# Kernel tuning notes

Measured on AMD Instinct MI355X. Metric: run time of the kernel, lower is better.

The kernel has to match this reference:

```python
import jax, jax.numpy as jnp
import numpy as np

N_NODES = 50000
N_EDGES = 800000
HID = 64
N_GRAPHS = 512
RATIO = 0.5
EPS = 1e-12


def setup_inputs() -> dict:
    key = jax.random.key(0)
    k1, k2, k3, k4, k5 = jax.random.split(key, 5)
    emb = jax.random.normal(k1, (N_NODES, HID), dtype=jnp.float32)
    edge_index = jax.random.randint(k2, (2, N_EDGES), 0, N_NODES, dtype=jnp.int32)
    batch = jnp.sort(jax.random.randint(k3, (N_NODES,), 0, N_GRAPHS, dtype=jnp.int32))
    W1 = jax.random.normal(k4, (2 * HID, 4 * HID), dtype=jnp.float32) * 0.05
    b1 = jnp.zeros((4 * HID,), dtype=jnp.float32)
    W2 = jax.random.normal(k5, (4 * HID, 1), dtype=jnp.float32) * 0.05
    b2 = jnp.zeros((1,), dtype=jnp.float32)
    return {"emb": emb, "edge_index": edge_index, "batch": batch,
            "W1": W1, "b1": b1, "W2": W2, "b2": b2}


def _relabel(edge_index, keep):
    # node_mask[v] = 1 iff v appears as endpoint of any kept edge
    flat = edge_index.reshape(-1)                       # [2E]
    keep2 = jnp.concatenate([keep, keep]).astype(jnp.int32)
    flag = jnp.zeros((N_NODES,), jnp.int32).at[flat].max(keep2)
    node_mask = flag > 0
    # compact new ids (torch: node_idx[sub_nodes] = arange(len(sub_nodes)))
    node_idx = jnp.where(node_mask, jnp.cumsum(node_mask.astype(jnp.int32)) - 1, -1)
    ei_rel = jnp.where(keep[None, :], node_idx[edge_index], -1)  # [2,E], -1 on dropped edges
    return ei_rel


def reference(emb, edge_index, batch, W1, b1, W2, b2):
    row, col = edge_index[0], edge_index[1]
    # edge MLP scoring: cat([emb[row], emb[col]]) -> Linear -> ReLU -> Linear -> scalar
    edge_rep = jnp.concatenate([emb[row], emb[col]], axis=-1)          # [E, 2H]
    h = jax.nn.relu(edge_rep @ W1 + b1)                                # [E, 4H]
    edge_att = (h @ W2 + b2).reshape(-1)                               # [E]

    # --- sparse_topk (descending) over segments index = batch[row] ---
    index = batch[row]                                                 # [E] graph id per edge
    f = edge_att
    fmin, fmax = f.min(), f.max()
    norm = (f - fmin) / (fmax - fmin + EPS) - index.astype(f.dtype)    # (-1)**descending = -1
    perm = jnp.argsort(-norm)                                          # descending sort
    ones = jnp.ones((N_EDGES,), jnp.int32)
    deg = jax.ops.segment_sum(ones, index, num_segments=N_GRAPHS)      # edges per graph
    k = jnp.ceil(RATIO * deg.astype(jnp.float32)).astype(jnp.int32)
    cum = jnp.cumsum(deg)
    start = cum - deg                                                  # start index of each graph block
    seg_sorted = index[perm]
    pos = jnp.arange(N_EDGES, dtype=jnp.int32)
    mask_sorted = (pos - start[seg_sorted]) < k[seg_sorted]            # top-k within each block
    keep = jnp.zeros((N_EDGES,), bool).at[perm].set(mask_sorted)       # causal edges, original order

    causal_edge_weight = jnp.where(keep, edge_att, 0.0)
    spu_edge_weight = jnp.where(keep, 0.0, -edge_att)

    causal_ei_rel = _relabel(edge_index, keep)
    spu_ei_rel = _relabel(edge_index, ~keep)

    scores = jnp.stack([edge_att, causal_edge_weight, spu_edge_weight])  # [3, E]
    return scores, causal_ei_rel, spu_ei_rel
```

## Files before the change

### kernel.cpp

```cpp
#include <hip/hip_runtime.h>
#include <hip/hip_bf16.h>
#include <stdint.h>

#define N_NODES 50000
#define N_EDGES 800000
#define N_GRAPHS 512
#define NSUB 16
#define NBUCK (N_GRAPHS * NSUB)

__device__ __forceinline__ unsigned f2sort(float f) {
    unsigned u = __float_as_uint(f);
    return (u & 0x80000000u) ? ~u : (u | 0x80000000u);
}
__device__ __forceinline__ float sort2f(unsigned u) {
    return __uint_as_float((u & 0x80000000u) ? (u ^ 0x80000000u) : ~u);
}

__global__ __launch_bounds__(256) void k0_count(const int* __restrict__ ei,
                                                const int* __restrict__ batch,
                                                unsigned* __restrict__ subdeg,
                                                int* __restrict__ node_start) {
    __shared__ unsigned hist[NBUCK];
    const int tid = threadIdx.x;
    for (int i = tid; i < NBUCK; i += 256) hist[i] = 0;
    __syncthreads();
    const int e0 = blockIdx.x * 4096;
    #pragma unroll 4
    for (int j = 0; j < 16; ++j) {
        int e = e0 + j * 256 + tid;
        if (e < N_EDGES) {
            int r = ei[e], c = ei[N_EDGES + e];
            atomicAdd(&hist[batch[r] * NSUB + (c >> 12)], 1u);
        }
    }
    #pragma unroll 4
    for (int j = 0; j < 16; ++j) {
        int i = e0 + j * 256 + tid;
        if (i < N_NODES) {
            int b = batch[i];
            if (i == 0) { for (int g2 = 0; g2 <= b; ++g2) node_start[g2] = 0; }
            else { int bp = batch[i - 1]; for (int g2 = bp + 1; g2 <= b; ++g2) node_start[g2] = i; }
            if (i == N_NODES - 1) { for (int g2 = b + 1; g2 <= N_GRAPHS; ++g2) node_start[g2] = N_NODES; }
        }
    }
    __syncthreads();
    for (int i = tid; i < NBUCK; i += 256) {
        unsigned h = hist[i];
        if (h) atomicAdd(&subdeg[i], h);
    }
}

__global__ __launch_bounds__(1024) void k3_scan(const unsigned* __restrict__ subdeg,
                                                unsigned* __restrict__ substart,
                                                unsigned* __restrict__ deg,
                                                unsigned* __restrict__ start,
                                                unsigned* __restrict__ kkv) {
    __shared__ unsigned lds[1024];
    const int t = threadIdx.x;
    unsigned v[8], s = 0;
    #pragma unroll
    for (int j = 0; j < 8; ++j) { v[j] = subdeg[t * 8 + j]; s += v[j]; }
    lds[t] = s;
    for (int off = 1; off < 1024; off <<= 1) {
        __syncthreads();
        unsigned u = (t >= off) ? lds[t - off] : 0u;
        __syncthreads();
        lds[t] += u;
    }
    __syncthreads();
    unsigned run = lds[t] - s;
    #pragma unroll
    for (int j = 0; j < 8; ++j) { substart[t * 8 + j] = run; run += v[j]; }
    if (t == 1023) substart[NBUCK] = lds[1023];
    __syncthreads();
    if (t < N_GRAPHS) {
        unsigned st0 = substart[t * NSUB];
        unsigned d = substart[(t + 1) * NSUB] - st0;
        start[t] = st0;
        deg[t] = d;
        kkv[t] = (d + 1u) >> 1;
    }
}

__global__ __launch_bounds__(256) void k4a_scatter(const int* __restrict__ ei,
                                                   const int* __restrict__ batch,
                                                   const unsigned* __restrict__ substart,
                                                   unsigned* __restrict__ subcursor,
                                                   unsigned* __restrict__ rcbuck,
                                                   unsigned* __restrict__ ebuck) {
    int e = blockIdx.x * 256 + threadIdx.x;
    int r = ei[e], c = ei[N_EDGES + e];
    int b = batch[r] * NSUB + (c >> 12);
    unsigned rank = atomicAdd(&subcursor[b], 1u);
    unsigned pos = substart[b] + rank;
    rcbuck[pos] = (unsigned)r | ((unsigned)c << 16);
    ebuck[pos]  = (unsigned)e;
}

__global__ __launch_bounds__(256) void k1_gemm(const float* __restrict__ emb,
                                               const float* __restrict__ W1,
                                               const float* __restrict__ b1,
                                               float* __restrict__ P,
                                               float* __restrict__ Q) {
    __shared__ float As[64][68];
    __shared__ float Bs[64][128];
    const int tid = threadIdx.x;
    const int v0  = blockIdx.x * 64;
    const int cy  = blockIdx.y;

    if (v0 + 64 <= N_NODES) {
        const float* srcA = emb + (size_t)v0 * 64;
        for (int idx = tid * 4; idx < 4096; idx += 1024) {
            float4 x = *(const float4*)(srcA + idx);
            int r = idx >> 6, k = idx & 63;
            As[k + 0][r] = x.x; As[k + 1][r] = x.y; As[k + 2][r] = x.z; As[k + 3][r] = x.w;
        }
    } else {
        for (int idx = tid * 4; idx < 4096; idx += 1024) {
            int r = idx >> 6, k = idx & 63;
            int v = v0 + r; if (v >= N_NODES) v = N_NODES - 1;
            float4 x = *(const float4*)(emb + (size_t)v * 64 + k);
            As[k + 0][r] = x.x; As[k + 1][r] = x.y; As[k + 2][r] = x.z; As[k + 3][r] = x.w;
        }
    }
    for (int idx = tid * 4; idx < 64 * 128; idx += 1024) {
        int k = idx >> 7, c = idx & 127;
        int jj = cy * 128 + c;
        const float* src = (jj < 256) ? (W1 + (size_t)k * 256 + jj)
                                      : (W1 + (size_t)(64 + k) * 256 + (jj - 256));
        *(float4*)&Bs[k][c] = *(const float4*)src;
    }
    __syncthreads();

    const int cgrp = tid & 31;
    const int rgrp = tid >> 5;
    float acc[8][4];
    #pragma unroll
    for (int r = 0; r < 8; ++r) { acc[r][0]=0.f; acc[r][1]=0.f; acc[r][2]=0.f; acc[r][3]=0.f; }

    #pragma unroll 8
    for (int k = 0; k < 64; ++k) {
        float4 b = *(const float4*)&Bs[k][cgrp * 4];
        const float4* ap = (const float4*)&As[k][rgrp * 8];
        float4 a01 = ap[0], a23 = ap[1];
        float av[8] = {a01.x, a01.y, a01.z, a01.w, a23.x, a23.y, a23.z, a23.w};
        #pragma unroll
        for (int r = 0; r < 8; ++r) {
            acc[r][0] = fmaf(av[r], b.x, acc[r][0]);
            acc[r][1] = fmaf(av[r], b.y, acc[r][1]);
            acc[r][2] = fmaf(av[r], b.z, acc[r][2]);
            acc[r][3] = fmaf(av[r], b.w, acc[r][3]);
        }
    }

    const int jj0 = cy * 128 + cgrp * 4;
    float4 badd = {0.f, 0.f, 0.f, 0.f};
    if (jj0 < 256) badd = *(const float4*)(b1 + jj0);
    #pragma unroll
    for (int r = 0; r < 8; ++r) {
        int v = v0 + rgrp * 8 + r;
        if (v < N_NODES) {
            float4 o = {acc[r][0] + badd.x, acc[r][1] + badd.y,
                        acc[r][2] + badd.z, acc[r][3] + badd.w};
            float* dst = (jj0 < 256) ? (P + (size_t)v * 256 + jj0)
                                     : (Q + (size_t)v * 256 + (jj0 - 256));
            *(float4*)dst = o;
        }
    }
}

__global__ __launch_bounds__(512, 4) void k2_edge(const float* __restrict__ P,
                                                  const float* __restrict__ Q,
                                                  const unsigned* __restrict__ rcbuck,
                                                  const unsigned* __restrict__ ebuck,
                                                  const unsigned* __restrict__ deg,
                                                  const unsigned* __restrict__ start,
                                                  const int* __restrict__ node_start,
                                                  const float* __restrict__ W2,
                                                  const float* __restrict__ b2,
                                                  float* __restrict__ att,
                                                  unsigned* __restrict__ minmax,
                                                  int ldsrows) {
    extern __shared__ float4 lds4[];
    const int g = blockIdx.x;
    const int n = (int)deg[g];
    if (n == 0) return;
    const int st = (int)start[g];
    const int n0 = node_start[g];
    const int nr = node_start[g + 1] - n0;
    const int ncap = nr < ldsrows ? nr : ldsrows;
    const int tid = threadIdx.x;

    const float4* Pg4 = (const float4*)(P + (size_t)n0 * 256);
    for (int u = tid; u < ncap * 64; u += 512) lds4[u] = Pg4[u];
    __syncthreads();

    const int lane = tid & 63;
    const int w = tid >> 6;
    const int j0 = lane * 4;
    const float4 w2v = *(const float4*)(W2 + j0);
    const float b2v = b2[0];
    float vmin = __builtin_inff(), vmax = -__builtin_inff();

    const int noct = (n + 7) >> 3;
    for (int oi = w; oi < noct; oi += 8) {
        const int i0 = st + oi * 8;
        int cnt = n - oi * 8; if (cnt > 8) cnt = 8;
        uint4 rcA = *(const uint4*)(rcbuck + i0);
        uint4 rcB = *(const uint4*)(rcbuck + i0 + 4);
        uint4 evA = *(const uint4*)(ebuck + i0);
        uint4 evB = *(const uint4*)(ebuck + i0 + 4);
        unsigned rc[8] = {rcA.x, rcA.y, rcA.z, rcA.w, rcB.x, rcB.y, rcB.z, rcB.w};
        unsigned ev[8] = {evA.x, evA.y, evA.z, evA.w, evB.x, evB.y, evB.z, evB.w};

        float4 p[8], q[8];
        #pragma unroll
        for (int j = 0; j < 8; ++j) {
            int r = (int)(rc[j] & 0xFFFFu);
            int c = (int)(rc[j] >> 16);
            int rl = r - n0;
            q[j] = *(const float4*)(Q + (size_t)c * 256 + j0);
            p[j] = (rl < ncap && rl >= 0) ? lds4[rl * 64 + lane]
                                          : *(const float4*)(P + (size_t)r * 256 + j0);
        }

        float part[8];
        #pragma unroll
        for (int j = 0; j < 8; ++j) {
            float s0 = fmaxf(p[j].x + q[j].x, 0.f);
            float s1 = fmaxf(p[j].y + q[j].y, 0.f);
            float s2 = fmaxf(p[j].z + q[j].z, 0.f);
            float s3 = fmaxf(p[j].w + q[j].w, 0.f);
            part[j] = fmaf(s3, w2v.w, fmaf(s2, w2v.z, fmaf(s1, w2v.y, s0 * w2v.x)));
        }
        #pragma unroll
        for (int off = 32; off; off >>= 1) {
            #pragma unroll
            for (int j = 0; j < 8; ++j) part[j] += __shfl_xor(part[j], off, 64);
        }
        float av = part[0]; unsigned ew = ev[0];
        #pragma unroll
        for (int j = 1; j < 8; ++j) if (lane == j) { av = part[j]; ew = ev[j]; }
        if (lane < cnt) att[ew] = av + b2v;

        #pragma unroll
        for (int j = 0; j < 8; ++j) {
            if (j < cnt) {
                float a = part[j] + b2v;
                vmin = fminf(vmin, a); vmax = fmaxf(vmax, a);
            }
        }
    }
    if (lane == 0) {
        atomicMin(&minmax[0], f2sort(vmin));
        atomicMax(&minmax[1], f2sort(vmax));
    }
}

__global__ __launch_bounds__(256) void k5_select(const unsigned* __restrict__ deg,
                                                 const unsigned* __restrict__ start,
                                                 const unsigned* __restrict__ kk,
                                                 const float* __restrict__ att,
                                                 const unsigned* __restrict__ ebuck,
                                                 const unsigned* __restrict__ rcbuck,
                                                 const unsigned* __restrict__ minmax,
                                                 unsigned char* __restrict__ keep,
                                                 unsigned char* __restrict__ flagC,
                                                 unsigned char* __restrict__ flagS) {
    __shared__ unsigned kbuf[4096];
    __shared__ unsigned hist[256];
    __shared__ unsigned sh_b, sh_excl, sh_cnt;
    const int g = blockIdx.x, t = threadIdx.x;
    int n = (int)deg[g]; if (n > 4096) n = 4096;
    if (n == 0) return;
    const unsigned st = start[g];
    const float fmin = sort2f(minmax[0]);
    const float fmax = sort2f(minmax[1]);
    const float denom = (fmax - fmin) + 1e-12f;
    const float gf = (float)g;
    for (int i = t; i < n; i += 256) {
        float a = att[ebuck[st + i]];
        float nq = (a - fmin) / denom;
        float mq = nq - gf;
        kbuf[i] = ~f2sort(mq);
    }
    const unsigned K = kk[g];

    unsigned lo = 0, prefix = 0, meq = 0;
    for (int byte = 3; byte >= 0; --byte) {
        __syncthreads();
        hist[t] = 0;
        __syncthreads();
        const int shAbove = (byte + 1) * 8;
        for (int i = t; i < n; i += 256) {
            unsigned k = kbuf[i];
            bool ok = (byte == 3) || ((k >> shAbove) == (prefix >> shAbove));
            if (ok) atomicAdd(&hist[(k >> (byte * 8)) & 0xFFu], 1u);
        }
        __syncthreads();
        unsigned v = hist[t];
        for (int off = 1; off < 256; off <<= 1) {
            __syncthreads();
            unsigned u = (t >= off) ? hist[t - off] : 0u;
            __syncthreads();
            hist[t] += u;
        }
        __syncthreads();
        unsigned incl = hist[t], excl = incl - v;
        unsigned target = K - lo;
        if (excl < target && target <= incl) { sh_b = (unsigned)t; sh_excl = excl; sh_cnt = v; }
        __syncthreads();
        prefix |= sh_b << (byte * 8);
        lo += sh_excl;
        meq = sh_cnt;
    }
    const unsigned T32 = prefix;
    const unsigned tneed = K - lo;
    bool keepAllTies = (tneed == meq);

    unsigned E_t = 0xFFFFFFFFu;
    if (!keepAllTies) {
        unsigned elo = 0, eprefix = 0;
        for (int byte = 2; byte >= 0; --byte) {
            __syncthreads();
            hist[t] = 0;
            __syncthreads();
            const int shAbove = (byte + 1) * 8;
            for (int i = t; i < n; i += 256) {
                if (kbuf[i] == T32) {
                    unsigned e = ebuck[st + i];
                    bool ok = (byte == 2) || ((e >> shAbove) == (eprefix >> shAbove));
                    if (ok) atomicAdd(&hist[(e >> (byte * 8)) & 0xFFu], 1u);
                }
            }
            __syncthreads();
            unsigned v = hist[t];
            for (int off = 1; off < 256; off <<= 1) {
                __syncthreads();
                unsigned u = (t >= off) ? hist[t - off] : 0u;
                __syncthreads();
                hist[t] += u;
            }
            __syncthreads();
            unsigned incl = hist[t], excl = incl - v;
            unsigned target = tneed - elo;
            if (excl < target && target <= incl) { sh_b = (unsigned)t; sh_excl = excl; }
            __syncthreads();
            eprefix |= sh_b << (byte * 8);
            elo += sh_excl;
        }
        E_t = eprefix;
    }

    __syncthreads();
    for (int i = t; i < n; i += 256) {
        unsigned k = kbuf[i];
        unsigned e = ebuck[st + i];
        bool kp = (k < T32) || (k == T32 && (keepAllTies || e <= E_t));
        keep[e] = kp ? 1 : 0;
        unsigned rc = rcbuck[st + i];
        int r = (int)(rc & 0xFFFFu), c = (int)(rc >> 16);
        if (kp) { flagC[r] = 1; flagC[c] = 1; }
        else    { flagS[r] = 1; flagS[c] = 1; }
    }
}

__global__ __launch_bounds__(1024) void k7_nodescan(const unsigned char* __restrict__ flagC,
                                                    const unsigned char* __restrict__ flagS,
                                                    int* __restrict__ nidxC,
                                                    int* __restrict__ nidxS) {
    const unsigned char* fl = blockIdx.x ? flagS : flagC;
    int* nx = blockIdx.x ? nidxS : nidxC;
    __shared__ int lds[1024];
    const int t = threadIdx.x;
    const int CH = (N_NODES + 1023) / 1024;
    const int base = t * CH;
    int s = 0;
    for (int i = 0; i < CH; ++i) { int v = base + i; if (v < N_NODES) s += fl[v]; }
    lds[t] = s;
    for (int off = 1; off < 1024; off <<= 1) {
        __syncthreads();
        int v = (t >= off) ? lds[t - off] : 0;
        __syncthreads();
        lds[t] += v;
    }
    __syncthreads();
    int run = lds[t] - s;
    for (int i = 0; i < CH; ++i) {
        int v = base + i;
        if (v < N_NODES) {
            if (fl[v]) { nx[v] = run; run++; } else nx[v] = -1;
        }
    }
}

__global__ __launch_bounds__(256) void k8_out(const float* __restrict__ att,
                                              const unsigned char* __restrict__ keep,
                                              const int* __restrict__ ei,
                                              const int* __restrict__ nidxC,
                                              const int* __restrict__ nidxS,
                                              float* __restrict__ out) {
    int e = blockIdx.x * 256 + threadIdx.x;
    float a = att[e];
    int kp = keep[e];
    int r = ei[e], c = ei[N_EDGES + e];
    out[e]               = a;
    out[N_EDGES + e]     = kp ? a : 0.f;
    out[2 * N_EDGES + e] = kp ? 0.f : -a;
    if (kp) {
        out[3 * N_EDGES + e] = (float)nidxC[r];
        out[4 * N_EDGES + e] = (float)nidxC[c];
        out[5 * N_EDGES + e] = -1.f;
        out[6 * N_EDGES + e] = -1.f;
    } else {
        out[3 * N_EDGES + e] = -1.f;
        out[4 * N_EDGES + e] = -1.f;
        out[5 * N_EDGES + e] = (float)nidxS[r];
        out[6 * N_EDGES + e] = (float)nidxS[c];
    }
}

extern "C" void kernel_launch(void* const* d_in, const int* in_sizes, int n_in,
                              void* d_out, int out_size, void* d_ws, size_t ws_size,
                              hipStream_t stream) {
    const float* emb   = (const float*)d_in[0];
    const int*   ei    = (const int*)d_in[1];
    const int*   batch = (const int*)d_in[2];
    const float* W1    = (const float*)d_in[3];
    const float* b1    = (const float*)d_in[4];
    const float* W2    = (const float*)d_in[5];
    const float* b2    = (const float*)d_in[6];
    float* out = (float*)d_out;

    char* ws = (char*)d_ws;
    size_t off = 0;
    auto alloc = [&](size_t bytes) -> void* {
        off = (off + 255) & ~(size_t)255;
        void* p = ws + off;
        off += bytes;
        return p;
    };

    float* P              = (float*)alloc((size_t)N_NODES * 256 * 4);
    float* Q              = (float*)alloc((size_t)N_NODES * 256 * 4);
    float* att            = (float*)alloc((size_t)N_EDGES * 4);
    unsigned* rcbuck      = (unsigned*)alloc(((size_t)N_EDGES + 8) * 4);
    unsigned* ebuck       = (unsigned*)alloc(((size_t)N_EDGES + 8) * 4);
    unsigned char* keep   = (unsigned char*)alloc(N_EDGES);
    unsigned char* flags2 = (unsigned char*)alloc((size_t)2 * N_NODES);
    unsigned char* flagC  = flags2;
    unsigned char* flagS  = flags2 + N_NODES;
    int* nidxC            = (int*)alloc((size_t)N_NODES * 4);
    int* nidxS            = (int*)alloc((size_t)N_NODES * 4);
    unsigned* meta        = (unsigned*)alloc((2 * NBUCK + 3 * 512 + 2) * 4);
    unsigned* subdeg      = meta;
    unsigned* subcursor   = meta + NBUCK;
    unsigned* deg         = meta + 2 * NBUCK;
    unsigned* start       = meta + 2 * NBUCK + 512;
    unsigned* kk          = meta + 2 * NBUCK + 1024;
    unsigned* minmax      = meta + 2 * NBUCK + 1536;
    unsigned* substart    = (unsigned*)alloc((NBUCK + 1) * 4);
    int* node_start       = (int*)alloc(513 * 4);

    const int EB = (N_EDGES + 255) / 256;
    const int SB = (N_EDGES + 4095) / 4096;

    hipMemsetAsync(meta, 0, (2 * NBUCK + 3 * 512 + 2) * 4, stream);
    hipMemsetAsync(minmax, 0xFF, 4, stream);
    hipMemsetAsync(flags2, 0, (size_t)2 * N_NODES, stream);

    int ldsrows = 78;
    if (hipFuncSetAttribute((const void*)k2_edge,
                            hipFuncAttributeMaxDynamicSharedMemorySize,
                            78 * 1024) != hipSuccess) {
        ldsrows = 56;
    }
    const size_t shbytes = (size_t)ldsrows * 1024;

    k0_count<<<SB, 256, 0, stream>>>(ei, batch, subdeg, node_start);
    k3_scan<<<1, 1024, 0, stream>>>(subdeg, substart, deg, start, kk);
    k4a_scatter<<<EB, 256, 0, stream>>>(ei, batch, substart, subcursor, rcbuck, ebuck);

    dim3 g1((N_NODES + 63) / 64, 4);
    k1_gemm<<<g1, 256, 0, stream>>>(emb, W1, b1, P, Q);

    k2_edge<<<N_GRAPHS, 512, shbytes, stream>>>(P, Q, rcbuck, ebuck, deg, start,
                                                node_start, W2, b2, att, minmax, ldsrows);

    k5_select<<<N_GRAPHS, 256, 0, stream>>>(deg, start, kk, att, ebuck, rcbuck,
                                            minmax, keep, flagC, flagS);
    k7_nodescan<<<2, 1024, 0, stream>>>(flagC, flagS, nidxC, nidxS);
    k8_out<<<EB, 256, 0, stream>>>(att, keep, ei, nidxC, nidxS, out);
}
```

Measured before the change: 407.6 us.

## Fuse count/scan/scatter and select/nodescan/output into persistent grid-barrier kernels

Merges the count, scan and scatter kernels into one kernel, and the select, node-scan and output kernels into another. Both use software grid barriers built on atomic counters, which cuts kernel launches and spreads the node scan across many blocks instead of two. It relies on every block being co-resident (196 and 512 blocks of 256 threads) without a cooperative launch, so it can deadlock if the GPU cannot schedule all blocks at once. It also resets the min/max inside the kernel rather than with a memset.

```diff
diff --git a/kernel.cpp b/kernel.cpp
--- a/kernel.cpp
+++ b/kernel.cpp
@@ -16,15 +16,35 @@
     return __uint_as_float((u & 0x80000000u) ? (u ^ 0x80000000u) : ~u);
 }
 
-__global__ __launch_bounds__(256) void k0_count(const int* __restrict__ ei,
-                                                const int* __restrict__ batch,
-                                                unsigned* __restrict__ subdeg,
-                                                int* __restrict__ node_start) {
+__device__ __forceinline__ void gridbar(unsigned* ctr, unsigned target) {
+    __syncthreads();
+    if (threadIdx.x == 0) {
+        __threadfence();
+        atomicAdd(ctr, 1u);
+        while (__hip_atomic_load(ctr, __ATOMIC_ACQUIRE, __HIP_MEMORY_SCOPE_AGENT) < target)
+            __builtin_amdgcn_s_sleep(2);
+    }
+    __syncthreads();
+}
+
+__global__ __launch_bounds__(256) void coopA(const int* __restrict__ ei,
+                                             const int* __restrict__ batch,
+                                             unsigned* __restrict__ subdeg,
+                                             unsigned* __restrict__ subcursor,
+                                             unsigned* __restrict__ substart,
+                                             int* __restrict__ node_start,
+                                             unsigned* __restrict__ minmax,
+                                             unsigned* __restrict__ bar,
+                                             unsigned* __restrict__ rcbuck,
+                                             unsigned* __restrict__ ebuck) {
     __shared__ unsigned hist[NBUCK];
+    __shared__ unsigned part[256];
     const int tid = threadIdx.x;
+    const int b   = blockIdx.x;
+    const int e0  = b * 4096;
+
     for (int i = tid; i < NBUCK; i += 256) hist[i] = 0;
     __syncthreads();
-    const int e0 = blockIdx.x * 4096;
     #pragma unroll 4
     for (int j = 0; j < 16; ++j) {
         int e = e0 + j * 256 + tid;
@@ -37,10 +57,10 @@
     for (int j = 0; j < 16; ++j) {
         int i = e0 + j * 256 + tid;
         if (i < N_NODES) {
-            int b = batch[i];
-            if (i == 0) { for (int g2 = 0; g2 <= b; ++g2) node_start[g2] = 0; }
-            else { int bp = batch[i - 1]; for (int g2 = bp + 1; g2 <= b; ++g2) node_start[g2] = i; }
-            if (i == N_NODES - 1) { for (int g2 = b + 1; g2 <= N_GRAPHS; ++g2) node_start[g2] = N_NODES; }
+            int bb = batch[i];
+            if (i == 0) { for (int g2 = 0; g2 <= bb; ++g2) node_start[g2] = 0; }
+            else { int bp = batch[i - 1]; for (int g2 = bp + 1; g2 <= bb; ++g2) node_start[g2] = i; }
+            if (i == N_NODES - 1) { for (int g2 = bb + 1; g2 <= N_GRAPHS; ++g2) node_start[g2] = N_NODES; }
         }
     }
     __syncthreads();
@@ -48,53 +68,42 @@
         unsigned h = hist[i];
         if (h) atomicAdd(&subdeg[i], h);
     }
-}
-
-__global__ __launch_bounds__(1024) void k3_scan(const unsigned* __restrict__ subdeg,
-                                                unsigned* __restrict__ substart,
-                                                unsigned* __restrict__ deg,
-                                                unsigned* __restrict__ start,
-                                                unsigned* __restrict__ kkv) {
-    __shared__ unsigned lds[1024];
-    const int t = threadIdx.x;
-    unsigned v[8], s = 0;
-    #pragma unroll
-    for (int j = 0; j < 8; ++j) { v[j] = subdeg[t * 8 + j]; s += v[j]; }
-    lds[t] = s;
-    for (int off = 1; off < 1024; off <<= 1) {
+    if (b == 0 && tid == 0) { minmax[0] = 0xFFFFFFFFu; minmax[1] = 0u; }
+    gridbar(bar + 0, gridDim.x);
+
+    if (b == 0) {
+        unsigned s = 0;
+        for (int j = 0; j < 32; ++j) s += subdeg[tid * 32 + j];
+        part[tid] = s;
+        for (int off = 1; off < 256; off <<= 1) {
+            __syncthreads();
+            unsigned u = (tid >= off) ? part[tid - off] : 0u;
+            __syncthreads();
+            part[tid] += u;
+        }
         __syncthreads();
-        unsigned u = (t >= off) ? lds[t - off] : 0u;
-        __syncthreads();
-        lds[t] += u;
-    }
-    __syncthreads();
-    unsigned run = lds[t] - s;
-    #pragma unroll
-    for (int j = 0; j < 8; ++j) { substart[t * 8 + j] = run; run += v[j]; }
-    if (t == 1023) substart[NBUCK] = lds[1023];
-    __syncthreads();
-    if (t < N_GRAPHS) {
-        unsigned st0 = substart[t * NSUB];
-        unsigned d = substart[(t + 1) * NSUB] - st0;
-        start[t] = st0;
-        deg[t] = d;
-        kkv[t] = (d + 1u) >> 1;
-    }
-}
-
-__global__ __launch_bounds__(256) void k4a_scatter(const int* __restrict__ ei,
-                                                   const int* __restrict__ batch,
-                                                   const unsigned* __restrict__ substart,
-                                                   unsigned* __restrict__ subcursor,
-                                                   unsigned* __restrict__ rcbuck,
-                                                   unsigned* __restrict__ ebuck) {
-    int e = blockIdx.x * 256 + threadIdx.x;
-    int r = ei[e], c = ei[N_EDGES + e];
-    int b = batch[r] * NSUB + (c >> 12);
-    unsigned rank = atomicAdd(&subcursor[b], 1u);
-    unsigned pos = substart[b] + rank;
-    rcbuck[pos] = (unsigned)r | ((unsigned)c << 16);
-    ebuck[pos]  = (unsigned)e;
+        unsigned run = part[tid] - s;
+        for (int j = 0; j < 32; ++j) {
+            unsigned d = subdeg[tid * 32 + j];
+            substart[tid * 32 + j] = run;
+            run += d;
+        }
+        if (tid == 255) substart[NBUCK] = run;
+    }
+    gridbar(bar + 1, gridDim.x);
+
+    #pragma unroll 4
+    for (int j = 0; j < 16; ++j) {
+        int e = e0 + j * 256 + tid;
+        if (e < N_EDGES) {
+            int r = ei[e], c = ei[N_EDGES + e];
+            int bk = batch[r] * NSUB + (c >> 12);
+            unsigned rank = atomicAdd(&subcursor[bk], 1u);
+            unsigned pos = substart[bk] + rank;
+            rcbuck[pos] = (unsigned)r | ((unsigned)c << 16);
+            ebuck[pos]  = (unsigned)e;
+        }
+    }
 }
 
 __global__ __launch_bounds__(256) void k1_gemm(const float* __restrict__ emb,
@@ -173,8 +182,7 @@
                                                   const float* __restrict__ Q,
                                                   const unsigned* __restrict__ rcbuck,
                                                   const unsigned* __restrict__ ebuck,
-                                                  const unsigned* __restrict__ deg,
-                                                  const unsigned* __restrict__ start,
+                                                  const unsigned* __restrict__ substart,
                                                   const int* __restrict__ node_start,
                                                   const float* __restrict__ W2,
                                                   const float* __restrict__ b2,
@@ -183,9 +191,9 @@
                                                   int ldsrows) {
     extern __shared__ float4 lds4[];
     const int g = blockIdx.x;
-    const int n = (int)deg[g];
+    const int st = (int)substart[g * NSUB];
+    const int n = (int)substart[(g + 1) * NSUB] - st;
     if (n == 0) return;
-    const int st = (int)start[g];
     const int n0 = node_start[g];
     const int nr = node_start[g + 1] - n0;
     const int ncap = nr < ldsrows ? nr : ldsrows;
@@ -257,166 +265,175 @@
     }
 }
 
-__global__ __launch_bounds__(256) void k5_select(const unsigned* __restrict__ deg,
-                                                 const unsigned* __restrict__ start,
-                                                 const unsigned* __restrict__ kk,
-                                                 const float* __restrict__ att,
-                                                 const unsigned* __restrict__ ebuck,
-                                                 const unsigned* __restrict__ rcbuck,
-                                                 const unsigned* __restrict__ minmax,
-                                                 unsigned char* __restrict__ keep,
-                                                 unsigned char* __restrict__ flagC,
-                                                 unsigned char* __restrict__ flagS) {
+__global__ __launch_bounds__(256) void coopB(const unsigned* __restrict__ substart,
+                                             const float* __restrict__ att,
+                                             const unsigned* __restrict__ ebuck,
+                                             const unsigned* __restrict__ rcbuck,
+                                             const unsigned* __restrict__ minmax,
+                                             const int* __restrict__ ei,
+                                             unsigned char* __restrict__ keep,
+                                             unsigned char* __restrict__ flagC,
+                                             unsigned char* __restrict__ flagS,
+                                             int* __restrict__ nidxC,
+                                             int* __restrict__ nidxS,
+                                             unsigned* __restrict__ partial,
+                                             unsigned* __restrict__ bar,
+                                             float* __restrict__ out) {
     __shared__ unsigned kbuf[4096];
     __shared__ unsigned hist[256];
     __shared__ unsigned sh_b, sh_excl, sh_cnt;
     const int g = blockIdx.x, t = threadIdx.x;
-    int n = (int)deg[g]; if (n > 4096) n = 4096;
-    if (n == 0) return;
-    const unsigned st = start[g];
-    const float fmin = sort2f(minmax[0]);
-    const float fmax = sort2f(minmax[1]);
-    const float denom = (fmax - fmin) + 1e-12f;
-    const float gf = (float)g;
-    for (int i = t; i < n; i += 256) {
-        float a = att[ebuck[st + i]];
-        float nq = (a - fmin) / denom;
-        float mq = nq - gf;
-        kbuf[i] = ~f2sort(mq);
-    }
-    const unsigned K = kk[g];
-
-    unsigned lo = 0, prefix = 0, meq = 0;
-    for (int byte = 3; byte >= 0; --byte) {
+    const unsigned st = substart[g * NSUB];
+    int n = (int)(substart[(g + 1) * NSUB] - st); if (n > 4096) n = 4096;
+
+    if (n > 0) {
+        const float fmin = sort2f(minmax[0]);
+        const float fmax = sort2f(minmax[1]);
+        const float denom = (fmax - fmin) + 1e-12f;
+        const float gf = (float)g;
+        for (int i = t; i < n; i += 256) {
+            float a = att[ebuck[st + i]];
+            float nq = (a - fmin) / denom;
+            float mq = nq - gf;
+            kbuf[i] = ~f2sort(mq);
+        }
+        const unsigned K = ((unsigned)n + 1u) >> 1;
+
+        unsigned lo = 0, prefix = 0, meq = 0;
+        for (int byte = 3; byte >= 0; --byte) {
+            __syncthreads();
+            hist[t] = 0;
+            __syncthreads();
+            const int shAbove = (byte + 1) * 8;
+            for (int i = t; i < n; i += 256) {
+                unsigned k = kbuf[i];
+                bool ok = (byte == 3) || ((k >> shAbove) == (prefix >> shAbove));
+                if (ok) atomicAdd(&hist[(k >> (byte * 8)) & 0xFFu], 1u);
+            }
+            __syncthreads();
+            unsigned v = hist[t];
+            for (int off = 1; off < 256; off <<= 1) {
+                __syncthreads();
+                unsigned u = (t >= off) ? hist[t - off] : 0u;
+                __syncthreads();
+                hist[t] += u;
+            }
+            __syncthreads();
+            unsigned incl = hist[t], excl = incl - v;
+            unsigned target = K - lo;
+            if (excl < target && target <= incl) { sh_b = (unsigned)t; sh_excl = excl; sh_cnt = v; }
+            __syncthreads();
+            prefix |= sh_b << (byte * 8);
+            lo += sh_excl;
+            meq = sh_cnt;
+        }
+        const unsigned T32 = prefix;
+        const unsigned tneed = K - lo;
+        bool keepAllTies = (tneed == meq);
+
+        unsigned E_t = 0xFFFFFFFFu;
+        if (!keepAllTies) {
+            unsigned elo = 0, eprefix = 0;
+            for (int byte = 2; byte >= 0; --byte) {
+                __syncthreads();
+                hist[t] = 0;
+                __syncthreads();
+                const int shAbove = (byte + 1) * 8;
+                for (int i = t; i < n; i += 256) {
+                    if (kbuf[i] == T32) {
+                        unsigned e = ebuck[st + i];
+                        bool ok = (byte == 2) || ((e >> shAbove) == (eprefix >> shAbove));
+                        if (ok) atomicAdd(&hist[(e >> (byte * 8)) & 0xFFu], 1u);
+                    }
+                }
+                __syncthreads();
+                unsigned v = hist[t];
+                for (int off = 1; off < 256; off <<= 1) {
+                    __syncthreads();
+                    unsigned u = (t >= off) ? hist[t - off] : 0u;
+                    __syncthreads();
+                    hist[t] += u;
+                }
+                __syncthreads();
+                unsigned incl = hist[t], excl = incl - v;
+                unsigned target = tneed - elo;
+                if (excl < target && target <= incl) { sh_b = (unsigned)t; sh_excl = excl; }
+                __syncthreads();
+                eprefix |= sh_b << (byte * 8);
+                elo += sh_excl;
+            }
+            E_t = eprefix;
+        }
+
         __syncthreads();
-        hist[t] = 0;
-        __syncthreads();
-        const int shAbove = (byte + 1) * 8;
         for (int i = t; i < n; i += 256) {
             unsigned k = kbuf[i];
-            bool ok = (byte == 3) || ((k >> shAbove) == (prefix >> shAbove));
-            if (ok) atomicAdd(&hist[(k >> (byte * 8)) & 0xFFu], 1u);
-        }
+            unsigned e = ebuck[st + i];
+            bool kp = (k < T32) || (k == T32 && (keepAllTies || e <= E_t));
+            keep[e] = kp ? 1 : 0;
+            unsigned rc = rcbuck[st + i];
+            int r = (int)(rc & 0xFFFFu), c = (int)(rc >> 16);
+            if (kp) { flagC[r] = 1; flagC[c] = 1; }
+            else    { flagS[r] = 1; flagS[c] = 1; }
+        }
+    }
+    gridbar(bar + 0, gridDim.x);
+
+    const int half = g >> 8;
+    const int bloc = g & 255;
+    const unsigned char* fl = half ? flagS : flagC;
+    int* nx = half ? nidxS : nidxC;
+    const int base = bloc * 196;
+    const int v = base + t;
+    const int f = (t < 196 && v < N_NODES) ? (int)fl[v] : 0;
+    __syncthreads();
+    hist[t] = (unsigned)f;
+    for (int off = 1; off < 256; off <<= 1) {
         __syncthreads();
-        unsigned v = hist[t];
-        for (int off = 1; off < 256; off <<= 1) {
-            __syncthreads();
-            unsigned u = (t >= off) ? hist[t - off] : 0u;
-            __syncthreads();
-            hist[t] += u;
-        }
+        unsigned u = (t >= off) ? hist[t - off] : 0u;
         __syncthreads();
-        unsigned incl = hist[t], excl = incl - v;
-        unsigned target = K - lo;
-        if (excl < target && target <= incl) { sh_b = (unsigned)t; sh_excl = excl; sh_cnt = v; }
+        hist[t] += u;
+    }
+    __syncthreads();
+    const unsigned exclL = hist[t] - (unsigned)f;
+    const unsigned totalMine = hist[255];
+    if (t == 0) partial[g] = totalMine;
+    gridbar(bar + 1, gridDim.x);
+
+    unsigned pv = partial[half * 256 + t];
+    __syncthreads();
+    hist[t] = pv;
+    for (int off = 1; off < 256; off <<= 1) {
         __syncthreads();
-        prefix |= sh_b << (byte * 8);
-        lo += sh_excl;
-        meq = sh_cnt;
-    }
-    const unsigned T32 = prefix;
-    const unsigned tneed = K - lo;
-    bool keepAllTies = (tneed == meq);
-
-    unsigned E_t = 0xFFFFFFFFu;
-    if (!keepAllTies) {
-        unsigned elo = 0, eprefix = 0;
-        for (int byte = 2; byte >= 0; --byte) {
-            __syncthreads();
-            hist[t] = 0;
-            __syncthreads();
-            const int shAbove = (byte + 1) * 8;
-            for (int i = t; i < n; i += 256) {
-                if (kbuf[i] == T32) {
-                    unsigned e = ebuck[st + i];
-                    bool ok = (byte == 2) || ((e >> shAbove) == (eprefix >> shAbove));
-                    if (ok) atomicAdd(&hist[(e >> (byte * 8)) & 0xFFu], 1u);
-                }
-            }
-            __syncthreads();
-            unsigned v = hist[t];
-            for (int off = 1; off < 256; off <<= 1) {
-                __syncthreads();
-                unsigned u = (t >= off) ? hist[t - off] : 0u;
-                __syncthreads();
-                hist[t] += u;
-            }
-            __syncthreads();
-            unsigned incl = hist[t], excl = incl - v;
-            unsigned target = tneed - elo;
-            if (excl < target && target <= incl) { sh_b = (unsigned)t; sh_excl = excl; }
-            __syncthreads();
-            eprefix |= sh_b << (byte * 8);
-            elo += sh_excl;
-        }
-        E_t = eprefix;
-    }
-
-    __syncthreads();
-    for (int i = t; i < n; i += 256) {
-        unsigned k = kbuf[i];
-        unsigned e = ebuck[st + i];
-        bool kp = (k < T32) || (k == T32 && (keepAllTies || e <= E_t));
-        keep[e] = kp ? 1 : 0;
-        unsigned rc = rcbuck[st + i];
-        int r = (int)(rc & 0xFFFFu), c = (int)(rc >> 16);
-        if (kp) { flagC[r] = 1; flagC[c] = 1; }
-        else    { flagS[r] = 1; flagS[c] = 1; }
-    }
-}
-
-__global__ __launch_bounds__(1024) void k7_nodescan(const unsigned char* __restrict__ flagC,
-                                                    const unsigned char* __restrict__ flagS,
-                                                    int* __restrict__ nidxC,
-                                                    int* __restrict__ nidxS) {
-    const unsigned char* fl = blockIdx.x ? flagS : flagC;
-    int* nx = blockIdx.x ? nidxS : nidxC;
-    __shared__ int lds[1024];
-    const int t = threadIdx.x;
-    const int CH = (N_NODES + 1023) / 1024;
-    const int base = t * CH;
-    int s = 0;
-    for (int i = 0; i < CH; ++i) { int v = base + i; if (v < N_NODES) s += fl[v]; }
-    lds[t] = s;
-    for (int off = 1; off < 1024; off <<= 1) {
+        unsigned u = (t >= off) ? hist[t - off] : 0u;
         __syncthreads();
-        int v = (t >= off) ? lds[t - off] : 0;
-        __syncthreads();
-        lds[t] += v;
-    }
-    __syncthreads();
-    int run = lds[t] - s;
-    for (int i = 0; i < CH; ++i) {
-        int v = base + i;
-        if (v < N_NODES) {
-            if (fl[v]) { nx[v] = run; run++; } else nx[v] = -1;
-        }
-    }
-}
-
-__global__ __launch_bounds__(256) void k8_out(const float* __restrict__ att,
-                                              const unsigned char* __restrict__ keep,
-                                              const int* __restrict__ ei,
-                                              const int* __restrict__ nidxC,
-                                              const int* __restrict__ nidxS,
-                                              float* __restrict__ out) {
-    int e = blockIdx.x * 256 + threadIdx.x;
-    float a = att[e];
-    int kp = keep[e];
-    int r = ei[e], c = ei[N_EDGES + e];
-    out[e]               = a;
-    out[N_EDGES + e]     = kp ? a : 0.f;
-    out[2 * N_EDGES + e] = kp ? 0.f : -a;
-    if (kp) {
-        out[3 * N_EDGES + e] = (float)nidxC[r];
-        out[4 * N_EDGES + e] = (float)nidxC[c];
-        out[5 * N_EDGES + e] = -1.f;
-        out[6 * N_EDGES + e] = -1.f;
-    } else {
-        out[3 * N_EDGES + e] = -1.f;
-        out[4 * N_EDGES + e] = -1.f;
-        out[5 * N_EDGES + e] = (float)nidxS[r];
-        out[6 * N_EDGES + e] = (float)nidxS[c];
+        hist[t] += u;
+    }
+    __syncthreads();
+    const unsigned baseOff = hist[bloc] - totalMine;
+    if (t < 196 && v < N_NODES) nx[v] = f ? (int)(baseOff + exclL) : -1;
+    gridbar(bar + 2, gridDim.x);
+
+    const int eb0 = g * 1563;
+    int eend = eb0 + 1563; if (eend > N_EDGES) eend = N_EDGES;
+    for (int e = eb0 + t; e < eend; e += 256) {
+        float a = att[e];
+        int kp = keep[e];
+        int r = ei[e], c = ei[N_EDGES + e];
+        out[e]               = a;
+        out[N_EDGES + e]     = kp ? a : 0.f;
+        out[2 * N_EDGES + e] = kp ? 0.f : -a;
+        if (kp) {
+            out[3 * N_EDGES + e] = (float)nidxC[r];
+            out[4 * N_EDGES + e] = (float)nidxC[c];
+            out[5 * N_EDGES + e] = -1.f;
+            out[6 * N_EDGES + e] = -1.f;
+        } else {
+            out[3 * N_EDGES + e] = -1.f;
+            out[4 * N_EDGES + e] = -1.f;
+            out[5 * N_EDGES + e] = (float)nidxS[r];
+            out[6 * N_EDGES + e] = (float)nidxS[c];
+        }
     }
 }
 
@@ -452,21 +469,18 @@
     unsigned char* flagS  = flags2 + N_NODES;
     int* nidxC            = (int*)alloc((size_t)N_NODES * 4);
     int* nidxS            = (int*)alloc((size_t)N_NODES * 4);
-    unsigned* meta        = (unsigned*)alloc((2 * NBUCK + 3 * 512 + 2) * 4);
+    unsigned* meta        = (unsigned*)alloc((2 * NBUCK + 2 + 8 + 512) * 4);
     unsigned* subdeg      = meta;
     unsigned* subcursor   = meta + NBUCK;
-    unsigned* deg         = meta + 2 * NBUCK;
-    unsigned* start       = meta + 2 * NBUCK + 512;
-    unsigned* kk          = meta + 2 * NBUCK + 1024;
-    unsigned* minmax      = meta + 2 * NBUCK + 1536;
+    unsigned* minmax      = meta + 2 * NBUCK;
+    unsigned* bar         = meta + 2 * NBUCK + 2;
+    unsigned* partial     = meta + 2 * NBUCK + 10;
     unsigned* substart    = (unsigned*)alloc((NBUCK + 1) * 4);
     int* node_start       = (int*)alloc(513 * 4);
 
-    const int EB = (N_EDGES + 255) / 256;
     const int SB = (N_EDGES + 4095) / 4096;
 
-    hipMemsetAsync(meta, 0, (2 * NBUCK + 3 * 512 + 2) * 4, stream);
-    hipMemsetAsync(minmax, 0xFF, 4, stream);
+    hipMemsetAsync(meta, 0, (2 * NBUCK + 2 + 8 + 512) * 4, stream);
     hipMemsetAsync(flags2, 0, (size_t)2 * N_NODES, stream);
 
     int ldsrows = 78;
@@ -477,18 +491,16 @@
     }
     const size_t shbytes = (size_t)ldsrows * 1024;
 
-    k0_count<<<SB, 256, 0, stream>>>(ei, batch, subdeg, node_start);
-    k3_scan<<<1, 1024, 0, stream>>>(subdeg, substart, deg, start, kk);
-    k4a_scatter<<<EB, 256, 0, stream>>>(ei, batch, substart, subcursor, rcbuck, ebuck);
+    coopA<<<SB, 256, 0, stream>>>(ei, batch, subdeg, subcursor, substart,
+                                  node_start, minmax, bar, rcbuck, ebuck);
 
     dim3 g1((N_NODES + 63) / 64, 4);
     k1_gemm<<<g1, 256, 0, stream>>>(emb, W1, b1, P, Q);
 
-    k2_edge<<<N_GRAPHS, 512, shbytes, stream>>>(P, Q, rcbuck, ebuck, deg, start,
+    k2_edge<<<N_GRAPHS, 512, shbytes, stream>>>(P, Q, rcbuck, ebuck, substart,
                                                 node_start, W2, b2, att, minmax, ldsrows);
 
-    k5_select<<<N_GRAPHS, 256, 0, stream>>>(deg, start, kk, att, ebuck, rcbuck,
-                                            minmax, keep, flagC, flagS);
-    k7_nodescan<<<2, 1024, 0, stream>>>(flagC, flagS, nidxC, nidxS);
-    k8_out<<<EB, 256, 0, stream>>>(att, keep, ei, nidxC, nidxS, out);
-}
+    coopB<<<N_GRAPHS, 256, 0, stream>>>(substart, att, ebuck, rcbuck, minmax, ei,
+                                        keep, flagC, flagS, nidxC, nidxS,
+                                        partial, bar + 4, out);
+}
```

New measurement: 583.4 us. 1.43x slower.

## Fold scan into count kernel and merge scatter with GEMM launch

Applied to the files above, without the earlier changes.

The bucket prefix scan now runs in the last-finishing block of the count kernel, detected with an atomic done counter, so the separate scan kernel is gone. The edge scatter shares one launch with the node GEMM: extra blocks past the GEMM range do the scatter, so the two independent jobs can overlap. The three memsets become one, and per-graph degree, start and k are derived from substart inside the consumer kernels. This cuts launch count and small-kernel serialisation, at the cost of a last-block pattern that relies on threadfence ordering.

```diff
diff --git a/kernel.cpp b/kernel.cpp
--- a/kernel.cpp
+++ b/kernel.cpp
@@ -7,6 +7,8 @@
 #define N_GRAPHS 512
 #define NSUB 16
 #define NBUCK (N_GRAPHS * NSUB)
+#define GEMM_BLOCKS 3128
+#define SCAT_BLOCKS 196
 
 __device__ __forceinline__ unsigned f2sort(float f) {
     unsigned u = __float_as_uint(f);
@@ -19,12 +21,17 @@
 __global__ __launch_bounds__(256) void k0_count(const int* __restrict__ ei,
                                                 const int* __restrict__ batch,
                                                 unsigned* __restrict__ subdeg,
-                                                int* __restrict__ node_start) {
+                                                unsigned* __restrict__ substart,
+                                                int* __restrict__ node_start,
+                                                unsigned* __restrict__ minmax,
+                                                unsigned* __restrict__ donecnt) {
     __shared__ unsigned hist[NBUCK];
+    __shared__ unsigned part[256];
+    __shared__ unsigned sh_last;
     const int tid = threadIdx.x;
+    const int e0 = blockIdx.x * 4096;
     for (int i = tid; i < NBUCK; i += 256) hist[i] = 0;
     __syncthreads();
-    const int e0 = blockIdx.x * 4096;
     #pragma unroll 4
     for (int j = 0; j < 16; ++j) {
         int e = e0 + j * 256 + tid;
@@ -48,65 +55,73 @@
         unsigned h = hist[i];
         if (h) atomicAdd(&subdeg[i], h);
     }
-}
-
-__global__ __launch_bounds__(1024) void k3_scan(const unsigned* __restrict__ subdeg,
-                                                unsigned* __restrict__ substart,
-                                                unsigned* __restrict__ deg,
-                                                unsigned* __restrict__ start,
-                                                unsigned* __restrict__ kkv) {
-    __shared__ unsigned lds[1024];
-    const int t = threadIdx.x;
-    unsigned v[8], s = 0;
-    #pragma unroll
-    for (int j = 0; j < 8; ++j) { v[j] = subdeg[t * 8 + j]; s += v[j]; }
-    lds[t] = s;
-    for (int off = 1; off < 1024; off <<= 1) {
-        __syncthreads();
-        unsigned u = (t >= off) ? lds[t - off] : 0u;
-        __syncthreads();
-        lds[t] += u;
-    }
-    __syncthreads();
-    unsigned run = lds[t] - s;
-    #pragma unroll
-    for (int j = 0; j < 8; ++j) { substart[t * 8 + j] = run; run += v[j]; }
-    if (t == 1023) substart[NBUCK] = lds[1023];
-    __syncthreads();
-    if (t < N_GRAPHS) {
-        unsigned st0 = substart[t * NSUB];
-        unsigned d = substart[(t + 1) * NSUB] - st0;
-        start[t] = st0;
-        deg[t] = d;
-        kkv[t] = (d + 1u) >> 1;
-    }
-}
-
-__global__ __launch_bounds__(256) void k4a_scatter(const int* __restrict__ ei,
-                                                   const int* __restrict__ batch,
-                                                   const unsigned* __restrict__ substart,
-                                                   unsigned* __restrict__ subcursor,
-                                                   unsigned* __restrict__ rcbuck,
-                                                   unsigned* __restrict__ ebuck) {
-    int e = blockIdx.x * 256 + threadIdx.x;
-    int r = ei[e], c = ei[N_EDGES + e];
-    int b = batch[r] * NSUB + (c >> 12);
-    unsigned rank = atomicAdd(&subcursor[b], 1u);
-    unsigned pos = substart[b] + rank;
-    rcbuck[pos] = (unsigned)r | ((unsigned)c << 16);
-    ebuck[pos]  = (unsigned)e;
-}
-
-__global__ __launch_bounds__(256) void k1_gemm(const float* __restrict__ emb,
-                                               const float* __restrict__ W1,
-                                               const float* __restrict__ b1,
-                                               float* __restrict__ P,
-                                               float* __restrict__ Q) {
+    if (tid == 0) {
+        minmax[0] = 0xFFFFFFFFu;
+        minmax[1] = 0u;
+        __threadfence();
+        sh_last = atomicAdd(donecnt, 1u);
+    }
+    __syncthreads();
+    if (sh_last != SCAT_BLOCKS - 1) return;
+    __threadfence();
+
+    unsigned v = 0;
+    {
+        unsigned s = 0;
+        unsigned loc[32];
+        #pragma unroll
+        for (int j = 0; j < 32; ++j) { loc[j] = subdeg[tid * 32 + j]; s += loc[j]; }
+        part[tid] = s;
+        for (int off = 1; off < 256; off <<= 1) {
+            __syncthreads();
+            unsigned u = (tid >= off) ? part[tid - off] : 0u;
+            __syncthreads();
+            part[tid] += u;
+        }
+        __syncthreads();
+        unsigned run = part[tid] - s;
+        #pragma unroll
+        for (int j = 0; j < 32; ++j) { substart[tid * 32 + j] = run; run += loc[j]; }
+        if (tid == 255) substart[NBUCK] = run;
+        v = run;
+    }
+    (void)v;
+}
+
+__global__ __launch_bounds__(256) void k14_gemm_scatter(const float* __restrict__ emb,
+                                                        const float* __restrict__ W1,
+                                                        const float* __restrict__ b1,
+                                                        float* __restrict__ P,
+                                                        float* __restrict__ Q,
+                                                        const int* __restrict__ ei,
+                                                        const int* __restrict__ batch,
+                                                        const unsigned* __restrict__ substart,
+                                                        unsigned* __restrict__ subcursor,
+                                                        unsigned* __restrict__ rcbuck,
+                                                        unsigned* __restrict__ ebuck) {
     __shared__ float As[64][68];
     __shared__ float Bs[64][128];
     const int tid = threadIdx.x;
-    const int v0  = blockIdx.x * 64;
-    const int cy  = blockIdx.y;
+
+    if (blockIdx.x >= GEMM_BLOCKS) {
+        const int e0 = (blockIdx.x - GEMM_BLOCKS) * 4096;
+        #pragma unroll 4
+        for (int j = 0; j < 16; ++j) {
+            int e = e0 + j * 256 + tid;
+            if (e < N_EDGES) {
+                int r = ei[e], c = ei[N_EDGES + e];
+                int bk = batch[r] * NSUB + (c >> 12);
+                unsigned rank = atomicAdd(&subcursor[bk], 1u);
+                unsigned pos = substart[bk] + rank;
+                rcbuck[pos] = (unsigned)r | ((unsigned)c << 16);
+                ebuck[pos]  = (unsigned)e;
+            }
+        }
+        return;
+    }
+
+    const int v0 = (blockIdx.x >> 2) * 64;
+    const int cy = blockIdx.x & 3;
 
     if (v0 + 64 <= N_NODES) {
         const float* srcA = emb + (size_t)v0 * 64;
@@ -173,8 +188,7 @@
                                                   const float* __restrict__ Q,
                                                   const unsigned* __restrict__ rcbuck,
                                                   const unsigned* __restrict__ ebuck,
-                                                  const unsigned* __restrict__ deg,
-                                                  const unsigned* __restrict__ start,
+                                                  const unsigned* __restrict__ substart,
                                                   const int* __restrict__ node_start,
                                                   const float* __restrict__ W2,
                                                   const float* __restrict__ b2,
@@ -183,9 +197,9 @@
                                                   int ldsrows) {
     extern __shared__ float4 lds4[];
     const int g = blockIdx.x;
-    const int n = (int)deg[g];
+    const int st = (int)substart[g * NSUB];
+    const int n = (int)substart[(g + 1) * NSUB] - st;
     if (n == 0) return;
-    const int st = (int)start[g];
     const int n0 = node_start[g];
     const int nr = node_start[g + 1] - n0;
     const int ncap = nr < ldsrows ? nr : ldsrows;
@@ -257,9 +271,7 @@
     }
 }
 
-__global__ __launch_bounds__(256) void k5_select(const unsigned* __restrict__ deg,
-                                                 const unsigned* __restrict__ start,
-                                                 const unsigned* __restrict__ kk,
+__global__ __launch_bounds__(256) void k5_select(const unsigned* __restrict__ substart,
                                                  const float* __restrict__ att,
                                                  const unsigned* __restrict__ ebuck,
                                                  const unsigned* __restrict__ rcbuck,
@@ -271,9 +283,9 @@
     __shared__ unsigned hist[256];
     __shared__ unsigned sh_b, sh_excl, sh_cnt;
     const int g = blockIdx.x, t = threadIdx.x;
-    int n = (int)deg[g]; if (n > 4096) n = 4096;
+    const unsigned st = substart[g * NSUB];
+    int n = (int)(substart[(g + 1) * NSUB] - st); if (n > 4096) n = 4096;
     if (n == 0) return;
-    const unsigned st = start[g];
     const float fmin = sort2f(minmax[0]);
     const float fmax = sort2f(minmax[1]);
     const float denom = (fmax - fmin) + 1e-12f;
@@ -284,7 +296,7 @@
         float mq = nq - gf;
         kbuf[i] = ~f2sort(mq);
     }
-    const unsigned K = kk[g];
+    const unsigned K = ((unsigned)n + 1u) >> 1;
 
     unsigned lo = 0, prefix = 0, meq = 0;
     for (int byte = 3; byte >= 0; --byte) {
@@ -447,27 +459,23 @@
     unsigned* rcbuck      = (unsigned*)alloc(((size_t)N_EDGES + 8) * 4);
     unsigned* ebuck       = (unsigned*)alloc(((size_t)N_EDGES + 8) * 4);
     unsigned char* keep   = (unsigned char*)alloc(N_EDGES);
-    unsigned char* flags2 = (unsigned char*)alloc((size_t)2 * N_NODES);
-    unsigned char* flagC  = flags2;
-    unsigned char* flagS  = flags2 + N_NODES;
     int* nidxC            = (int*)alloc((size_t)N_NODES * 4);
     int* nidxS            = (int*)alloc((size_t)N_NODES * 4);
-    unsigned* meta        = (unsigned*)alloc((2 * NBUCK + 3 * 512 + 2) * 4);
+    const size_t zero_words = 2 * NBUCK + 1 + 2;
+    const size_t zero_bytes = zero_words * 4 + (size_t)2 * N_NODES;
+    unsigned* meta        = (unsigned*)alloc(zero_bytes);
     unsigned* subdeg      = meta;
     unsigned* subcursor   = meta + NBUCK;
-    unsigned* deg         = meta + 2 * NBUCK;
-    unsigned* start       = meta + 2 * NBUCK + 512;
-    unsigned* kk          = meta + 2 * NBUCK + 1024;
-    unsigned* minmax      = meta + 2 * NBUCK + 1536;
+    unsigned* donecnt     = meta + 2 * NBUCK;
+    unsigned* minmax      = meta + 2 * NBUCK + 1;
+    unsigned char* flagC  = (unsigned char*)(meta + zero_words);
+    unsigned char* flagS  = flagC + N_NODES;
     unsigned* substart    = (unsigned*)alloc((NBUCK + 1) * 4);
     int* node_start       = (int*)alloc(513 * 4);
 
     const int EB = (N_EDGES + 255) / 256;
-    const int SB = (N_EDGES + 4095) / 4096;
-
-    hipMemsetAsync(meta, 0, (2 * NBUCK + 3 * 512 + 2) * 4, stream);
-    hipMemsetAsync(minmax, 0xFF, 4, stream);
-    hipMemsetAsync(flags2, 0, (size_t)2 * N_NODES, stream);
+
+    hipMemsetAsync(meta, 0, zero_bytes, stream);
 
     int ldsrows = 78;
     if (hipFuncSetAttribute((const void*)k2_edge,
@@ -477,17 +485,16 @@
     }
     const size_t shbytes = (size_t)ldsrows * 1024;
 
-    k0_count<<<SB, 256, 0, stream>>>(ei, batch, subdeg, node_start);
-    k3_scan<<<1, 1024, 0, stream>>>(subdeg, substart, deg, start, kk);
-    k4a_scatter<<<EB, 256, 0, stream>>>(ei, batch, substart, subcursor, rcbuck, ebuck);
-
-    dim3 g1((N_NODES + 63) / 64, 4);
-    k1_gemm<<<g1, 256, 0, stream>>>(emb, W1, b1, P, Q);
-
-    k2_edge<<<N_GRAPHS, 512, shbytes, stream>>>(P, Q, rcbuck, ebuck, deg, start,
+    k0_count<<<SCAT_BLOCKS, 256, 0, stream>>>(ei, batch, subdeg, substart,
+                                              node_start, minmax, donecnt);
+
+    k14_gemm_scatter<<<GEMM_BLOCKS + SCAT_BLOCKS, 256, 0, stream>>>(
+        emb, W1, b1, P, Q, ei, batch, substart, subcursor, rcbuck, ebuck);
+
+    k2_edge<<<N_GRAPHS, 512, shbytes, stream>>>(P, Q, rcbuck, ebuck, substart,
                                                 node_start, W2, b2, att, minmax, ldsrows);
 
-    k5_select<<<N_GRAPHS, 256, 0, stream>>>(deg, start, kk, att, ebuck, rcbuck,
+    k5_select<<<N_GRAPHS, 256, 0, stream>>>(substart, att, ebuck, rcbuck,
                                             minmax, keep, flagC, flagS);
     k7_nodescan<<<2, 1024, 0, stream>>>(flagC, flagS, nidxC, nidxS);
     k8_out<<<EB, 256, 0, stream>>>(att, keep, ei, nidxC, nidxS, out);
```

New measurement: 426.6 us. 1.05x slower.
